# Performance work log

Hardware: AMD Instinct MI355X
Metric: run time of the kernel (lower is better)

The kernel has to match this reference:

```python
import jax, jax.numpy as jnp
import numpy as np

HIDDEN = 1024
HEADS = 16
HEAD_DIM = HIDDEN // HEADS  # 64
BATCH = 2
SEQ = 2048
MASK_IDENTITY = True


def setup_inputs() -> dict:
    key = jax.random.key(0)
    ks = jax.random.split(key, 9)
    s = 1.0 / np.sqrt(HIDDEN)
    return {
        "hidden_states": jax.random.normal(ks[0], (BATCH, SEQ, HIDDEN), jnp.float32),
        "Wq": jax.random.normal(ks[1], (HIDDEN, HIDDEN), jnp.float32) * s,
        "bq": jnp.zeros((HIDDEN,), jnp.float32),
        "Wk": jax.random.normal(ks[2], (HIDDEN, HIDDEN), jnp.float32) * s,
        "bk": jnp.zeros((HIDDEN,), jnp.float32),
        "Wv": jax.random.normal(ks[3], (HIDDEN, HIDDEN), jnp.float32) * s,
        "bv": jnp.zeros((HIDDEN,), jnp.float32),
        "Wd": jax.random.normal(ks[4], (HIDDEN, HIDDEN), jnp.float32) * s,
        "bd": jnp.zeros((HIDDEN,), jnp.float32),
    }


def _split_heads(x):
    # [B, S, H*Dh] -> [B, H, S, Dh]
    b, s, _ = x.shape
    return x.reshape(b, s, HEADS, HEAD_DIM).transpose(0, 2, 1, 3)


def reference(hidden_states, Wq, bq, Wk, bk, Wv, bv, Wd, bd):
    # torch Linear: y = x @ W.T + b
    q = _split_heads(hidden_states @ Wq.T + bq)  # [B,H,S,Dh]
    k = _split_heads(hidden_states @ Wk.T + bk)
    v = _split_heads(hidden_states @ Wv.T + bv)

    scores = jnp.einsum("bhqd,bhkd->bhqk", q, k) / np.sqrt(HEAD_DIM)
    if MASK_IDENTITY:
        mask_value = -jnp.finfo(scores.dtype).max
        eye = jnp.eye(scores.shape[-1], dtype=bool)  # [S,S], broadcast over B,H
        scores = jnp.where(eye, mask_value, scores)
    probs = jax.nn.softmax(scores, axis=-1)
    ctx = jnp.einsum("bhqk,bhkd->bhqd", probs, v)  # [B,H,S,Dh]
    b, h, s, d = ctx.shape
    ctx = ctx.transpose(0, 2, 1, 3).reshape(b, s, h * d)  # [B,S,H*Dh]
    return ctx @ Wd.T + bd
```

## Files before the change

kernel.cpp:

```cpp
#include <hip/hip_runtime.h>
#include <hip/hip_bf16.h>
#include <stdint.h>

#define HIDDEN 1024
#define SEQL   2048
#define NB     2
#define NH     16
#define DH     64
#define MTOT   (NB * SEQL)
#define QKVLD  3072
#define SCALE_Q 0.18033688011112042f

typedef __bf16 bf16x8 __attribute__((ext_vector_type(8)));
typedef __bf16 bf16x4 __attribute__((ext_vector_type(4)));
typedef float  f32x4  __attribute__((ext_vector_type(4)));
typedef float  f32x16 __attribute__((ext_vector_type(16)));

__device__ __forceinline__ void gload16(const void* g, void* l) {
    __builtin_amdgcn_global_load_lds(
        (const __attribute__((address_space(1))) void*)g,
        (__attribute__((address_space(3))) void*)l, 16, 0, 0);
}
__device__ __forceinline__ float exp2fast(float x) {
    float r;
    asm("v_exp_f32 %0, %1" : "=v"(r) : "v"(x));
    return r;
}
__device__ __forceinline__ unsigned cvtpk(float lo, float hi) {
    unsigned r;
    asm("v_cvt_pk_bf16_f32 %0, %1, %2" : "=v"(r) : "v"(lo), "v"(hi));
    return r;
}
__device__ __forceinline__ void pswap(unsigned& a, unsigned& b) {
    asm volatile("v_permlane32_swap_b32 %0, %1" : "+v"(a), "+v"(b));
}

__global__ void cvt_f32_bf16(const float* __restrict__ src,
                             __bf16* __restrict__ dst, int n4) {
    int i = blockIdx.x * blockDim.x + threadIdx.x;
    if (i < n4) {
        float4 v = reinterpret_cast<const float4*>(src)[i];
        bf16x4 o = { (__bf16)v.x, (__bf16)v.y, (__bf16)v.z, (__bf16)v.w };
        reinterpret_cast<bf16x4*>(dst)[i] = o;
    }
}

__global__ void cvt_w4(const float* __restrict__ Wq, const float* __restrict__ Wk,
                       const float* __restrict__ Wv, const float* __restrict__ Wd,
                       __bf16* __restrict__ dst) {
    int seg = blockIdx.y;
    const float* src = seg == 0 ? Wq : seg == 1 ? Wk : seg == 2 ? Wv : Wd;
    float sc = (seg == 0) ? SCALE_Q : 1.0f;
    int i = blockIdx.x * 256 + threadIdx.x;
    float4 v = reinterpret_cast<const float4*>(src)[i];
    bf16x4 o = { (__bf16)(v.x * sc), (__bf16)(v.y * sc),
                 (__bf16)(v.z * sc), (__bf16)(v.w * sc) };
    reinterpret_cast<bf16x4*>(dst)[(size_t)seg * 262144 + i] = o;
}

__global__ void pack_bias(const float* __restrict__ bq, const float* __restrict__ bk,
                          const float* __restrict__ bv, float* __restrict__ dst) {
    int i = blockIdx.x * 256 + threadIdx.x;
    float v = (i < 1024) ? bq[i] * SCALE_Q : (i < 2048) ? bk[i - 1024] : bv[i - 2048];
    dst[i] = v;
}

__global__ __launch_bounds__(256) void transpose_v(const __bf16* __restrict__ QKV,
                                                   __bf16* __restrict__ Vt) {
    __shared__ __bf16 t[64][66];
    const int st = blockIdx.x, bh = blockIdx.y;
    const int b = bh >> 4, h = bh & 15;
    const int tid = threadIdx.x;
    const int r = tid >> 3, c = tid & 7;
    const __bf16* src = QKV + (size_t)(b * SEQL + st * 64) * QKVLD + 2048 + h * 64;
    *(int4*)&t[r][c * 8]      = *(const int4*)(src + (size_t)r * QKVLD + c * 8);
    *(int4*)&t[r + 32][c * 8] = *(const int4*)(src + (size_t)(r + 32) * QKVLD + c * 8);
    __syncthreads();
    __bf16* dst = Vt + (size_t)bh * DH * SEQL + st * 64;
    const int d = tid >> 3;
    __bf16 tmp0[8], tmp1[8];
#pragma unroll
    for (int j = 0; j < 8; ++j) {
        tmp0[j] = t[c * 8 + j][d];
        tmp1[j] = t[c * 8 + j][d + 32];
    }
    *(int4*)(dst + (size_t)d * SEQL + c * 8)        = *(int4*)tmp0;
    *(int4*)(dst + (size_t)(d + 32) * SEQL + c * 8) = *(int4*)tmp1;
}

__global__ __launch_bounds__(256) void gemm_qkv(const __bf16* __restrict__ A,
                                                const __bf16* __restrict__ Bw,
                                                const float* __restrict__ bias,
                                                __bf16* __restrict__ C) {
    __shared__ __bf16 As[128 * 32];
    __shared__ __bf16 Bs[128 * 32];
    const int K = 1024, N = QKVLD;

    int bid = blockIdx.x;
    int swz = (bid & 7) * 96 + (bid >> 3);
    const int bm = (swz & 31) * 128;
    const int bn = (swz >> 5) * 128;

    const int tid = threadIdx.x;
    const int w = tid >> 6, l = tid & 63, g = l >> 4, lc = l & 15;
    const int wr = (w >> 1) * 64, wc = (w & 1) * 64;
    const int row = tid >> 2, ch = tid & 3;

    const __bf16* Ap = A  + (size_t)(bm + row) * K + ch * 8;
    const __bf16* Bp = Bw + (size_t)(bn + row) * K + ch * 8;
    __bf16* AsLo = &As[w * 512];
    __bf16* AsHi = &As[2048 + w * 512];
    __bf16* BsLo = &Bs[w * 512];
    __bf16* BsHi = &Bs[2048 + w * 512];

    f32x4 acc[4][4];
    const f32x4 z4 = {0.f, 0.f, 0.f, 0.f};
#pragma unroll
    for (int i = 0; i < 4; ++i)
#pragma unroll
        for (int j = 0; j < 4; ++j) acc[i][j] = z4;

    for (int kt = 0; kt < K; kt += 32) {
        gload16(Ap + kt,                   AsLo);
        gload16(Ap + kt + (size_t)64 * K,  AsHi);
        gload16(Bp + kt,                   BsLo);
        gload16(Bp + kt + (size_t)64 * K,  BsHi);
        __syncthreads();

        bf16x8 af[4], bfr[4];
#pragma unroll
        for (int i = 0; i < 4; ++i)
            af[i] = *(const bf16x8*)&As[(wr + i * 16 + lc) * 32 + g * 8];
#pragma unroll
        for (int j = 0; j < 4; ++j)
            bfr[j] = *(const bf16x8*)&Bs[(wc + j * 16 + lc) * 32 + g * 8];
        __builtin_amdgcn_s_setprio(1);
#pragma unroll
        for (int i = 0; i < 4; ++i)
#pragma unroll
            for (int j = 0; j < 4; ++j)
                acc[i][j] = __builtin_amdgcn_mfma_f32_16x16x32_bf16(af[i], bfr[j], acc[i][j], 0, 0, 0);
        __builtin_amdgcn_s_setprio(0);
        __syncthreads();
    }

#pragma unroll
    for (int i = 0; i < 4; ++i) {
        int r0 = bm + wr + i * 16 + g * 4;
#pragma unroll
        for (int j = 0; j < 4; ++j) {
            int c = bn + wc + j * 16 + lc;
            float bb = bias[c];
#pragma unroll
            for (int r = 0; r < 4; ++r)
                C[(size_t)(r0 + r) * N + c] = (__bf16)(acc[i][j][r] + bb);
        }
    }
}

__global__ __launch_bounds__(256) void gemm_out(const __bf16* __restrict__ A,
                                                const __bf16* __restrict__ Bw,
                                                const float* __restrict__ bias,
                                                float* __restrict__ Cout) {
    __shared__ __bf16 As[128 * 32];
    __shared__ __bf16 Bs[128 * 32];
    const int M = MTOT, N = HIDDEN, K = HIDDEN;

    const int tid = threadIdx.x;
    const int w = tid >> 6, l = tid & 63, g = l >> 4, lc = l & 15;
    const int wr = (w >> 1) * 64, wc = (w & 1) * 64;
    const int bm = blockIdx.x * 128, bn = blockIdx.y * 128;
    const int row = tid >> 2, ch = tid & 3;

    const __bf16* Arow0 = A  + (size_t)(bm + row) * K + ch * 8;
    const __bf16* Arow1 = Arow0 + (size_t)64 * K;
    const __bf16* Brow0 = Bw + (size_t)(bn + row) * K + ch * 8;
    const __bf16* Brow1 = Brow0 + (size_t)64 * K;

    f32x4 acc[4][4];
    const f32x4 z4 = {0.f, 0.f, 0.f, 0.f};
#pragma unroll
    for (int i = 0; i < 4; ++i)
#pragma unroll
        for (int j = 0; j < 4; ++j) acc[i][j] = z4;

    int4 ra0 = *(const int4*)(Arow0);
    int4 ra1 = *(const int4*)(Arow1);
    int4 rb0 = *(const int4*)(Brow0);
    int4 rb1 = *(const int4*)(Brow1);

    for (int kt = 0; kt < K; kt += 32) {
        *(int4*)&As[row * 32 + ch * 8]        = ra0;
        *(int4*)&As[(64 + row) * 32 + ch * 8] = ra1;
        *(int4*)&Bs[row * 32 + ch * 8]        = rb0;
        *(int4*)&Bs[(64 + row) * 32 + ch * 8] = rb1;
        __syncthreads();

        if (kt + 32 < K) {
            ra0 = *(const int4*)(Arow0 + kt + 32);
            ra1 = *(const int4*)(Arow1 + kt + 32);
            rb0 = *(const int4*)(Brow0 + kt + 32);
            rb1 = *(const int4*)(Brow1 + kt + 32);
        }

        bf16x8 af[4], bfr[4];
#pragma unroll
        for (int i = 0; i < 4; ++i)
            af[i] = *(const bf16x8*)&As[(wr + i * 16 + lc) * 32 + g * 8];
#pragma unroll
        for (int j = 0; j < 4; ++j)
            bfr[j] = *(const bf16x8*)&Bs[(wc + j * 16 + lc) * 32 + g * 8];
        __builtin_amdgcn_s_setprio(1);
#pragma unroll
        for (int i = 0; i < 4; ++i)
#pragma unroll
            for (int j = 0; j < 4; ++j)
                acc[i][j] = __builtin_amdgcn_mfma_f32_16x16x32_bf16(af[i], bfr[j], acc[i][j], 0, 0, 0);
        __builtin_amdgcn_s_setprio(0);
        __syncthreads();
    }

#pragma unroll
    for (int i = 0; i < 4; ++i) {
        int r0 = bm + wr + i * 16 + g * 4;
#pragma unroll
        for (int j = 0; j < 4; ++j) {
            int c = bn + wc + j * 16 + lc;
            float bb = bias[c];
#pragma unroll
            for (int r = 0; r < 4; ++r)
                Cout[(size_t)(r0 + r) * N + c] = acc[i][j][r] + bb;
        }
    }
}

__global__ __launch_bounds__(256) void attn_kernel(const __bf16* __restrict__ QKV,
                                                   const __bf16* __restrict__ Vt,
                                                   __bf16* __restrict__ Ctx) {
    __shared__ __bf16 k_lds[2][64][64];
    __shared__ __bf16 v_lds[2][64][64];
    __shared__ float  bc[4][32];

    const int tid = threadIdx.x;
    const int w  = tid >> 6;
    const int l  = tid & 63;
    const int ql = l & 31;
    const int lh = l >> 5;

    int bid = blockIdx.x;
    int swz = (bid & 7) * 64 + (bid >> 3);
    const int qt = swz & 15, bh = swz >> 4;
    const int b = bh >> 4, hd = bh & 15;
    const int qw = qt * 128 + w * 32;

    const __bf16* Qg = QKV + (size_t)b * SEQL * QKVLD + hd * DH;
    const __bf16* Kg = Qg + 1024;
    const __bf16* Vg = Vt + (size_t)bh * DH * SEQL;

    bf16x8 qf[4];
    {
        const __bf16* qp = Qg + (size_t)(qw + ql) * QKVLD + lh * 8;
#pragma unroll
        for (int c = 0; c < 4; ++c) qf[c] = *(const bf16x8*)(qp + c * 16);
    }

    const int sr   = l >> 3;
    const int gcol = ((l & 7) * 8) ^ (sr << 3);
    auto stage = [&](int kb, int nb) {
        const __bf16* kp = Kg + (size_t)(kb + w * 8 + sr) * QKVLD + gcol;
        const __bf16* vp = Vg + (size_t)(w * 8 + sr) * SEQL + kb + gcol;
        gload16(kp,                          &k_lds[nb][w * 8][0]);
        gload16(kp + (size_t)32 * QKVLD,     &k_lds[nb][32 + w * 8][0]);
        gload16(vp,                          &v_lds[nb][w * 8][0]);
        gload16(vp + (size_t)32 * SEQL,      &v_lds[nb][32 + w * 8][0]);
    };

    stage(0, 0);
    __syncthreads();

    f32x16 o0, o1;
#pragma unroll
    for (int r = 0; r < 16; ++r) { o0[r] = 0.f; o1[r] = 0.f; }
    float m_r = -1e30f, l_r = 0.f;

    const int NT = SEQL / 64;
    const int rsw = (ql & 7) << 3;

    for (int kt = 0; kt < NT; ++kt) {
        const int buf = kt & 1;
        const int kb = kt * 64;

        if (kt + 1 < NT) stage(kb + 64, buf ^ 1);

        f32x16 sA, sB;
#pragma unroll
        for (int r = 0; r < 16; ++r) { sA[r] = 0.f; sB[r] = 0.f; }
        __builtin_amdgcn_s_setprio(1);
#pragma unroll
        for (int c = 0; c < 4; ++c) {
            bf16x8 k0 = *(const bf16x8*)&k_lds[buf][ql]     [(c * 16 + lh * 8) ^ rsw];
            bf16x8 k1 = *(const bf16x8*)&k_lds[buf][32 + ql][(c * 16 + lh * 8) ^ rsw];
            sA = __builtin_amdgcn_mfma_f32_32x32x16_bf16(k0, qf[c], sA, 0, 0, 0);
            sB = __builtin_amdgcn_mfma_f32_32x32x16_bf16(k1, qf[c], sB, 0, 0, 0);
        }
        __builtin_amdgcn_s_setprio(0);

        float p[32];
#pragma unroll
        for (int r = 0; r < 16; ++r) { p[r] = sA[r]; p[16 + r] = sB[r]; }

        if (kb < qw + 32 && qw < kb + 64) {
            const int qg = qw + ql;
#pragma unroll
            for (int i = 0; i < 32; ++i) {
                int kg = kb + ((i >> 4) << 5) + (i & 3) + ((i >> 2) & 3) * 8 + lh * 4;
                if (kg == qg) p[i] = -1e30f;
            }
        }

        float t16[16];
#pragma unroll
        for (int i = 0; i < 16; ++i) t16[i] = fmaxf(p[i], p[i + 16]);
#pragma unroll
        for (int i = 0; i < 8; ++i) t16[i] = fmaxf(t16[i], t16[i + 8]);
#pragma unroll
        for (int i = 0; i < 4; ++i) t16[i] = fmaxf(t16[i], t16[i + 4]);
        float pm = fmaxf(fmaxf(t16[0], t16[1]), fmaxf(t16[2], t16[3]));
        pm = fmaxf(pm, __shfl_xor(pm, 32, 64));

        if (__any(pm > m_r + 8.f)) {
            float mn = fmaxf(m_r, pm);
            float al = exp2fast(m_r - mn);
            m_r = mn;
            l_r *= al;
            if (lh == 0) bc[w][ql] = al;
            asm volatile("s_waitcnt lgkmcnt(0)" ::: "memory");
            float ag[16];
#pragma unroll
            for (int r = 0; r < 16; ++r)
                ag[r] = bc[w][(r & 3) + (r >> 2) * 8 + lh * 4];
#pragma unroll
            for (int r = 0; r < 16; ++r) { o0[r] *= ag[r]; o1[r] *= ag[r]; }
        }

#pragma unroll
        for (int i = 0; i < 32; ++i) p[i] = exp2fast(p[i] - m_r);
        float s16[16];
#pragma unroll
        for (int i = 0; i < 16; ++i) s16[i] = p[i] + p[i + 16];
#pragma unroll
        for (int i = 0; i < 8; ++i) s16[i] += s16[i + 8];
#pragma unroll
        for (int i = 0; i < 4; ++i) s16[i] += s16[i + 4];
        float rs = (s16[0] + s16[1]) + (s16[2] + s16[3]);
        rs += __shfl_xor(rs, 32, 64);
        l_r += rs;

        bf16x8 pa[4];
#pragma unroll
        for (int s = 0; s < 2; ++s) {
            unsigned w0 = cvtpk(p[s * 16 + 0],  p[s * 16 + 1]);
            unsigned w1 = cvtpk(p[s * 16 + 2],  p[s * 16 + 3]);
            unsigned w2 = cvtpk(p[s * 16 + 4],  p[s * 16 + 5]);
            unsigned w3 = cvtpk(p[s * 16 + 6],  p[s * 16 + 7]);
            unsigned w4 = cvtpk(p[s * 16 + 8],  p[s * 16 + 9]);
            unsigned w5 = cvtpk(p[s * 16 + 10], p[s * 16 + 11]);
            unsigned w6 = cvtpk(p[s * 16 + 12], p[s * 16 + 13]);
            unsigned w7 = cvtpk(p[s * 16 + 14], p[s * 16 + 15]);
            pswap(w0, w2); pswap(w1, w3);
            pswap(w4, w6); pswap(w5, w7);
            uint4 lo4 = {w0, w1, w2, w3};
            uint4 hi4 = {w4, w5, w6, w7};
            pa[s * 2 + 0] = *(bf16x8*)&lo4;
            pa[s * 2 + 1] = *(bf16x8*)&hi4;
        }

        __builtin_amdgcn_s_setprio(1);
#pragma unroll
        for (int s = 0; s < 2; ++s)
#pragma unroll
            for (int sl = 0; sl < 2; ++sl) {
                const int col = s * 32 + sl * 16 + lh * 8;
                bf16x8 v0 = *(const bf16x8*)&v_lds[buf][ql]     [col ^ rsw];
                bf16x8 v1 = *(const bf16x8*)&v_lds[buf][32 + ql][col ^ rsw];
                o0 = __builtin_amdgcn_mfma_f32_32x32x16_bf16(pa[s * 2 + sl], v0, o0, 0, 0, 0);
                o1 = __builtin_amdgcn_mfma_f32_32x32x16_bf16(pa[s * 2 + sl], v1, o1, 0, 0, 0);
            }
        __builtin_amdgcn_s_setprio(0);

        __syncthreads();
    }

    if (lh == 0) bc[w][ql] = 1.f / l_r;
    asm volatile("s_waitcnt lgkmcnt(0)" ::: "memory");
#pragma unroll
    for (int r = 0; r < 16; ++r) {
        int cr = (r & 3) + (r >> 2) * 8 + lh * 4;
        float iv = bc[w][cr];
        int qrow = qw + cr;
        __bf16* cp = Ctx + (size_t)(b * SEQL + qrow) * HIDDEN + hd * DH + ql;
        cp[0]  = (__bf16)(o0[r] * iv);
        cp[32] = (__bf16)(o1[r] * iv);
    }
}

extern "C" void kernel_launch(void* const* d_in, const int* in_sizes, int n_in,
                              void* d_out, int out_size, void* d_ws, size_t ws_size,
                              hipStream_t stream) {
    const float* H  = (const float*)d_in[0];
    const float* Wq = (const float*)d_in[1];
    const float* bq = (const float*)d_in[2];
    const float* Wk = (const float*)d_in[3];
    const float* bk = (const float*)d_in[4];
    const float* Wv = (const float*)d_in[5];
    const float* bv = (const float*)d_in[6];
    const float* Wd = (const float*)d_in[7];
    const float* bd = (const float*)d_in[8];
    float* out = (float*)d_out;

    char* ws = (char*)d_ws;
    const size_t MB = 1024 * 1024;
    __bf16* Hb    = (__bf16*)(ws + 0 * MB);
    __bf16* Ctx   = (__bf16*)(ws + 0 * MB);
    __bf16* Wqkvb = (__bf16*)(ws + 8 * MB);
    __bf16* Wdb   = (__bf16*)(ws + 14 * MB);
    float*  bqkv  = (float*) (ws + 16 * MB);
    __bf16* QKV   = (__bf16*)(ws + 17 * MB);
    __bf16* Vtb   = (__bf16*)(ws + 41 * MB);
    if (ws_size < 49 * MB) return;

    cvt_f32_bf16<<<4096, 256, 0, stream>>>(H, Hb, MTOT * HIDDEN / 4);
    cvt_w4<<<dim3(1024, 4), 256, 0, stream>>>(Wq, Wk, Wv, Wd, Wqkvb);
    pack_bias<<<12, 256, 0, stream>>>(bq, bk, bv, bqkv);

    gemm_qkv<<<768, 256, 0, stream>>>(Hb, Wqkvb, bqkv, QKV);

    transpose_v<<<dim3(32, 32), 256, 0, stream>>>(QKV, Vtb);

    attn_kernel<<<512, 256, 0, stream>>>(QKV, Vtb, Ctx);

    gemm_out<<<dim3(32, 8), 256, 0, stream>>>(Ctx, Wdb, bd, out);
}
```

Measured before the change: 137.4 us.

## Split attention over key range in two halves and merge partial results

```diff
diff --git a/kernel.cpp b/kernel.cpp
--- a/kernel.cpp
+++ b/kernel.cpp
@@ -10,6 +10,8 @@
 #define MTOT   (NB * SEQL)
 #define QKVLD  3072
 #define SCALE_Q 0.18033688011112042f
+#define SPLITS 2
+#define KSPAN  (SEQL / SPLITS)
 
 typedef __bf16 bf16x8 __attribute__((ext_vector_type(8)));
 typedef __bf16 bf16x4 __attribute__((ext_vector_type(4)));
@@ -164,7 +166,7 @@
                                                 float* __restrict__ Cout) {
     __shared__ __bf16 As[128 * 32];
     __shared__ __bf16 Bs[128 * 32];
-    const int M = MTOT, N = HIDDEN, K = HIDDEN;
+    const int N = HIDDEN, K = HIDDEN;
 
     const int tid = threadIdx.x;
     const int w = tid >> 6, l = tid & 63, g = l >> 4, lc = l & 15;
@@ -236,7 +238,9 @@
 
 __global__ __launch_bounds__(256) void attn_kernel(const __bf16* __restrict__ QKV,
                                                    const __bf16* __restrict__ Vt,
-                                                   __bf16* __restrict__ Ctx) {
+                                                   __bf16* __restrict__ P0,
+                                                   __bf16* __restrict__ P1,
+                                                   float2* __restrict__ ML) {
     __shared__ __bf16 k_lds[2][64][64];
     __shared__ __bf16 v_lds[2][64][64];
     __shared__ float  bc[4][32];
@@ -248,14 +252,17 @@
     const int lh = l >> 5;
 
     int bid = blockIdx.x;
-    int swz = (bid & 7) * 64 + (bid >> 3);
-    const int qt = swz & 15, bh = swz >> 4;
+    int swz = (bid & 7) * 128 + (bid >> 3);
+    const int split = swz >> 9;
+    const int qt = swz & 15, bh = (swz >> 4) & 31;
     const int b = bh >> 4, hd = bh & 15;
     const int qw = qt * 128 + w * 32;
+    const int koff = split * KSPAN;
 
     const __bf16* Qg = QKV + (size_t)b * SEQL * QKVLD + hd * DH;
     const __bf16* Kg = Qg + 1024;
     const __bf16* Vg = Vt + (size_t)bh * DH * SEQL;
+    __bf16* Pg = split ? P1 : P0;
 
     bf16x8 qf[4];
     {
@@ -275,7 +282,7 @@
         gload16(vp + (size_t)32 * SEQL,      &v_lds[nb][32 + w * 8][0]);
     };
 
-    stage(0, 0);
+    stage(koff, 0);
     __syncthreads();
 
     f32x16 o0, o1;
@@ -283,12 +290,12 @@
     for (int r = 0; r < 16; ++r) { o0[r] = 0.f; o1[r] = 0.f; }
     float m_r = -1e30f, l_r = 0.f;
 
-    const int NT = SEQL / 64;
+    const int NT = KSPAN / 64;
     const int rsw = (ql & 7) << 3;
 
     for (int kt = 0; kt < NT; ++kt) {
         const int buf = kt & 1;
-        const int kb = kt * 64;
+        const int kb = koff + kt * 64;
 
         if (kt + 1 < NT) stage(kb + 64, buf ^ 1);
 
@@ -391,17 +398,38 @@
         __syncthreads();
     }
 
-    if (lh == 0) bc[w][ql] = 1.f / l_r;
-    asm volatile("s_waitcnt lgkmcnt(0)" ::: "memory");
+    if (lh == 0) ML[(size_t)split * 65536 + bh * 2048 + qw + ql] = make_float2(m_r, l_r);
 #pragma unroll
     for (int r = 0; r < 16; ++r) {
         int cr = (r & 3) + (r >> 2) * 8 + lh * 4;
-        float iv = bc[w][cr];
         int qrow = qw + cr;
-        __bf16* cp = Ctx + (size_t)(b * SEQL + qrow) * HIDDEN + hd * DH + ql;
-        cp[0]  = (__bf16)(o0[r] * iv);
-        cp[32] = (__bf16)(o1[r] * iv);
-    }
+        __bf16* cp = Pg + (size_t)(b * SEQL + qrow) * HIDDEN + hd * DH + ql;
+        cp[0]  = (__bf16)o0[r];
+        cp[32] = (__bf16)o1[r];
+    }
+}
+
+__global__ __launch_bounds__(256) void attn_merge(const __bf16* __restrict__ P1,
+                                                  const float2* __restrict__ ML,
+                                                  __bf16* __restrict__ Ctx ) {
+    int idx = blockIdx.x * 256 + threadIdx.x;
+    int e = idx * 8;
+    int row = e >> 10, col = e & 1023;
+    int q = row & (SEQL - 1), b = row >> 11, hd = col >> 6;
+    size_t bhq = (size_t)(b * 16 + hd) * 2048 + q;
+    float2 t0 = ML[bhq];
+    float2 t1 = ML[65536 + bhq];
+    float M = fmaxf(t0.x, t1.x);
+    float a0 = exp2fast(t0.x - M), a1 = exp2fast(t1.x - M);
+    float inv = 1.f / (a0 * t0.y + a1 * t1.y);
+    a0 *= inv; a1 *= inv;
+    bf16x8 u0 = reinterpret_cast<const bf16x8*>(Ctx)[idx];
+    bf16x8 u1 = reinterpret_cast<const bf16x8*>(P1)[idx];
+    bf16x8 o;
+#pragma unroll
+    for (int j = 0; j < 8; ++j)
+        o[j] = (__bf16)((float)u0[j] * a0 + (float)u1[j] * a1);
+    reinterpret_cast<bf16x8*>(Ctx)[idx] = o;
 }
 
 extern "C" void kernel_launch(void* const* d_in, const int* in_sizes, int n_in,
@@ -427,7 +455,9 @@
     float*  bqkv  = (float*) (ws + 16 * MB);
     __bf16* QKV   = (__bf16*)(ws + 17 * MB);
     __bf16* Vtb   = (__bf16*)(ws + 41 * MB);
-    if (ws_size < 49 * MB) return;
+    __bf16* P1    = (__bf16*)(ws + 49 * MB);
+    float2* ML    = (float2*)(ws + 57 * MB);
+    if (ws_size < 58 * MB) return;
 
     cvt_f32_bf16<<<4096, 256, 0, stream>>>(H, Hb, MTOT * HIDDEN / 4);
     cvt_w4<<<dim3(1024, 4), 256, 0, stream>>>(Wq, Wk, Wv, Wd, Wqkvb);
@@ -437,7 +467,8 @@
 
     transpose_v<<<dim3(32, 32), 256, 0, stream>>>(QKV, Vtb);
 
-    attn_kernel<<<512, 256, 0, stream>>>(QKV, Vtb, Ctx);
+    attn_kernel<<<1024, 256, 0, stream>>>(QKV, Vtb, Ctx, P1, ML);
+    attn_merge<<<2048, 256, 0, stream>>>(P1, ML, Ctx);
 
     gemm_out<<<dim3(32, 8), 256, 0, stream>>>(Ctx, Wdb, bd, out);
 }
```

New measurement: 144.5 us. +5.2%, slower.

## Load attention K/V tiles directly into registers instead of LDS staging

Applied to the files above, without the earlier changes.

```diff
diff --git a/kernel.cpp b/kernel.cpp
--- a/kernel.cpp
+++ b/kernel.cpp
@@ -164,7 +164,7 @@
                                                 float* __restrict__ Cout) {
     __shared__ __bf16 As[128 * 32];
     __shared__ __bf16 Bs[128 * 32];
-    const int M = MTOT, N = HIDDEN, K = HIDDEN;
+    const int N = HIDDEN, K = HIDDEN;
 
     const int tid = threadIdx.x;
     const int w = tid >> 6, l = tid & 63, g = l >> 4, lc = l & 15;
@@ -237,9 +237,7 @@
 __global__ __launch_bounds__(256) void attn_kernel(const __bf16* __restrict__ QKV,
                                                    const __bf16* __restrict__ Vt,
                                                    __bf16* __restrict__ Ctx) {
-    __shared__ __bf16 k_lds[2][64][64];
-    __shared__ __bf16 v_lds[2][64][64];
-    __shared__ float  bc[4][32];
+    __shared__ float bc[4][32];
 
     const int tid = threadIdx.x;
     const int w  = tid >> 6;
@@ -264,19 +262,9 @@
         for (int c = 0; c < 4; ++c) qf[c] = *(const bf16x8*)(qp + c * 16);
     }
 
-    const int sr   = l >> 3;
-    const int gcol = ((l & 7) * 8) ^ (sr << 3);
-    auto stage = [&](int kb, int nb) {
-        const __bf16* kp = Kg + (size_t)(kb + w * 8 + sr) * QKVLD + gcol;
-        const __bf16* vp = Vg + (size_t)(w * 8 + sr) * SEQL + kb + gcol;
-        gload16(kp,                          &k_lds[nb][w * 8][0]);
-        gload16(kp + (size_t)32 * QKVLD,     &k_lds[nb][32 + w * 8][0]);
-        gload16(vp,                          &v_lds[nb][w * 8][0]);
-        gload16(vp + (size_t)32 * SEQL,      &v_lds[nb][32 + w * 8][0]);
-    };
-
-    stage(0, 0);
-    __syncthreads();
+    const __bf16* kp  = Kg + (size_t)ql * QKVLD + lh * 8;
+    const __bf16* vp0 = Vg + (size_t)ql * SEQL + lh * 8;
+    const __bf16* vp1 = Vg + (size_t)(32 + ql) * SEQL + lh * 8;
 
     f32x16 o0, o1;
 #pragma unroll
@@ -284,13 +272,19 @@
     float m_r = -1e30f, l_r = 0.f;
 
     const int NT = SEQL / 64;
-    const int rsw = (ql & 7) << 3;
+
+    bf16x8 kf[8];
+    {
+        const __bf16* kpt = kp;
+#pragma unroll
+        for (int c = 0; c < 4; ++c) {
+            kf[c]     = *(const bf16x8*)(kpt + c * 16);
+            kf[4 + c] = *(const bf16x8*)(kpt + (size_t)32 * QKVLD + c * 16);
+        }
+    }
 
     for (int kt = 0; kt < NT; ++kt) {
-        const int buf = kt & 1;
         const int kb = kt * 64;
-
-        if (kt + 1 < NT) stage(kb + 64, buf ^ 1);
 
         f32x16 sA, sB;
 #pragma unroll
@@ -298,12 +292,26 @@
         __builtin_amdgcn_s_setprio(1);
 #pragma unroll
         for (int c = 0; c < 4; ++c) {
-            bf16x8 k0 = *(const bf16x8*)&k_lds[buf][ql]     [(c * 16 + lh * 8) ^ rsw];
-            bf16x8 k1 = *(const bf16x8*)&k_lds[buf][32 + ql][(c * 16 + lh * 8) ^ rsw];
-            sA = __builtin_amdgcn_mfma_f32_32x32x16_bf16(k0, qf[c], sA, 0, 0, 0);
-            sB = __builtin_amdgcn_mfma_f32_32x32x16_bf16(k1, qf[c], sB, 0, 0, 0);
+            sA = __builtin_amdgcn_mfma_f32_32x32x16_bf16(kf[c],     qf[c], sA, 0, 0, 0);
+            sB = __builtin_amdgcn_mfma_f32_32x32x16_bf16(kf[4 + c], qf[c], sB, 0, 0, 0);
         }
         __builtin_amdgcn_s_setprio(0);
+
+        if (kt + 1 < NT) {
+            const __bf16* kpt = kp + (size_t)(kb + 64) * QKVLD;
+#pragma unroll
+            for (int c = 0; c < 4; ++c) {
+                kf[c]     = *(const bf16x8*)(kpt + c * 16);
+                kf[4 + c] = *(const bf16x8*)(kpt + (size_t)32 * QKVLD + c * 16);
+            }
+        }
+
+        bf16x8 vf[8];
+#pragma unroll
+        for (int j = 0; j < 4; ++j) {
+            vf[j]     = *(const bf16x8*)(vp0 + kb + j * 16);
+            vf[4 + j] = *(const bf16x8*)(vp1 + kb + j * 16);
+        }
 
         float p[32];
 #pragma unroll
@@ -318,14 +326,13 @@
             }
         }
 
-        float t16[16];
-#pragma unroll
-        for (int i = 0; i < 16; ++i) t16[i] = fmaxf(p[i], p[i + 16]);
-#pragma unroll
-        for (int i = 0; i < 8; ++i) t16[i] = fmaxf(t16[i], t16[i + 8]);
-#pragma unroll
-        for (int i = 0; i < 4; ++i) t16[i] = fmaxf(t16[i], t16[i + 4]);
-        float pm = fmaxf(fmaxf(t16[0], t16[1]), fmaxf(t16[2], t16[3]));
+        float t8[8];
+#pragma unroll
+        for (int i = 0; i < 8; ++i)
+            t8[i] = fmaxf(fmaxf(p[i], p[i + 8]), fmaxf(p[i + 16], p[i + 24]));
+#pragma unroll
+        for (int i = 0; i < 4; ++i) t8[i] = fmaxf(t8[i], t8[i + 4]);
+        float pm = fmaxf(fmaxf(t8[0], t8[1]), fmaxf(t8[2], t8[3]));
         pm = fmaxf(pm, __shfl_xor(pm, 32, 64));
 
         if (__any(pm > m_r + 8.f)) {
@@ -345,14 +352,13 @@
 
 #pragma unroll
         for (int i = 0; i < 32; ++i) p[i] = exp2fast(p[i] - m_r);
-        float s16[16];
-#pragma unroll
-        for (int i = 0; i < 16; ++i) s16[i] = p[i] + p[i + 16];
-#pragma unroll
-        for (int i = 0; i < 8; ++i) s16[i] += s16[i + 8];
-#pragma unroll
-        for (int i = 0; i < 4; ++i) s16[i] += s16[i + 4];
-        float rs = (s16[0] + s16[1]) + (s16[2] + s16[3]);
+        float s8[8];
+#pragma unroll
+        for (int i = 0; i < 8; ++i)
+            s8[i] = (p[i] + p[i + 8]) + (p[i + 16] + p[i + 24]);
+#pragma unroll
+        for (int i = 0; i < 4; ++i) s8[i] += s8[i + 4];
+        float rs = (s8[0] + s8[1]) + (s8[2] + s8[3]);
         rs += __shfl_xor(rs, 32, 64);
         l_r += rs;
 
@@ -377,18 +383,11 @@
 
         __builtin_amdgcn_s_setprio(1);
 #pragma unroll
-        for (int s = 0; s < 2; ++s)
-#pragma unroll
-            for (int sl = 0; sl < 2; ++sl) {
-                const int col = s * 32 + sl * 16 + lh * 8;
-                bf16x8 v0 = *(const bf16x8*)&v_lds[buf][ql]     [col ^ rsw];
-                bf16x8 v1 = *(const bf16x8*)&v_lds[buf][32 + ql][col ^ rsw];
-                o0 = __builtin_amdgcn_mfma_f32_32x32x16_bf16(pa[s * 2 + sl], v0, o0, 0, 0, 0);
-                o1 = __builtin_amdgcn_mfma_f32_32x32x16_bf16(pa[s * 2 + sl], v1, o1, 0, 0, 0);
-            }
+        for (int j = 0; j < 4; ++j) {
+            o0 = __builtin_amdgcn_mfma_f32_32x32x16_bf16(pa[j], vf[j],     o0, 0, 0, 0);
+            o1 = __builtin_amdgcn_mfma_f32_32x32x16_bf16(pa[j], vf[4 + j], o1, 0, 0, 0);
+        }
         __builtin_amdgcn_s_setprio(0);
-
-        __syncthreads();
     }
 
     if (lh == 0) bc[w][ql] = 1.f / l_r;
```

New measurement: 191.4 us. +39.3%, slower.
